# Optimization experiments

Measured on AMD Instinct MI355X. Metric: run time of the kernel, lower is better.

Reference implementation:

```python
import jax, jax.numpy as jnp
import numpy as np

K = 16          # num neighbor samples
SHARE = 8       # share_planes


def _conv1x1(x, w, b=None):
    # x: [B, Cin, N, K], w: [Cout, Cin]
    y = jnp.einsum('oc,bcnk->bonk', w, x)
    if b is not None:
        y = y + b[None, :, None, None]
    return y


def setup_inputs() -> dict:
    key = jax.random.key(0)
    ks = jax.random.split(key, 18)
    B, CIN, N = 4, 64, 16384
    MID, OUT, PT = 64, 128, 8
    s = 0.05  # weight scale

    def w(k, shape):
        return jax.random.normal(k, shape, jnp.float32) * s

    return {
        'sm_feats': jax.random.normal(ks[0], (B, CIN, N, K), jnp.float32),
        'sm_ppfs': jax.random.normal(ks[1], (B, PT, N, K), jnp.float32),
        'w0': w(ks[2], (OUT, CIN)),   'b0': w(ks[3], (OUT,)),
        'w1': w(ks[4], (MID, OUT)),   'b1': w(ks[5], (MID,)),
        'w2': w(ks[6], (MID, OUT)),   'b2': w(ks[7], (MID,)),
        'w3': w(ks[8], (MID, OUT)),   'b3': w(ks[9], (MID,)),
        'pw1': w(ks[10], (MID, PT)),
        'pw2': w(ks[11], (MID, MID)),
        'cw1': w(ks[12], (MID // SHARE, MID * K)),
        'cw2': w(ks[13], (K * MID // SHARE, MID // SHARE)), 'cb2': w(ks[14], (K * MID // SHARE,)),
        'wout': w(ks[15], (OUT, MID)), 'bout': w(ks[16], (OUT,)),
    }


def reference(sm_feats, sm_ppfs, w0, b0, w1, b1, w2, b2, w3, b3,
              pw1, pw2, cw1, cw2, cb2, wout, bout):
    B, _, N, k = sm_feats.shape
    xn = jax.nn.relu(_conv1x1(sm_feats, w0, b0))          # [B, OUT, N, K]
    x = xn[:, :, :, 0:1]                                   # [B, OUT, N, 1]
    identity = x
    x1 = _conv1x1(x, w1, b1)                               # [B, MID, N, 1]
    x2 = _conv1x1(xn, w2, b2)                              # [B, MID, N, K]
    x3 = _conv1x1(xn, w3, b3)                              # [B, MID, N, K]
    ptf = _conv1x1(jax.nn.relu(_conv1x1(sm_ppfs, pw1)), pw2)  # [B, MID, N, K]
    x3 = x3 + ptf
    xfs = x1 - x2 + ptf                                    # [B, MID, N, K]
    mid = xfs.shape[1]
    # transpose(2,3).view(B, MID*K, 1, N)
    xfs = jnp.transpose(xfs, (0, 1, 3, 2)).reshape(B, mid * k, 1, N)
    h = jax.nn.relu(_conv1x1(xfs, cw1))                    # [B, MID//S, 1, N]
    wl = _conv1x1(h, cw2, cb2)                             # [B, K*MID//S, 1, N]
    wl = wl.reshape(B, mid // SHARE, k, N)
    w = jax.nn.softmax(wl, axis=2)                         # softmax over K samples
    w = jnp.transpose(w, (0, 1, 3, 2))                     # [B, MID//S, N, K]
    w = jnp.tile(w, (1, SHARE, 1, 1))                      # [B, MID, N, K]
    out = jax.nn.relu(jnp.sum(w * x3, axis=3, keepdims=True))  # [B, MID, N, 1]
    out = _conv1x1(out, wout, bout) + identity             # [B, OUT, N, 1]
    return out[:, :, :, 0]                                 # [B, OUT, N]
```

## Files before the change

kernel.cpp:

```cpp
#include <hip/hip_runtime.h>
#include <stdint.h>

typedef unsigned int uint32;
typedef __attribute__((ext_vector_type(4))) float f32x4;
typedef __attribute__((ext_vector_type(4))) uint32 u32x4;
typedef __attribute__((ext_vector_type(8))) short bf16x8;

#define NPOS_TOTAL 65536
#define WPB 4
#define POS_PER_WAVE 32
#define NBLOCKS 512
#define CSTRIDE 262144

#define OFF_AW0 0
#define OFF_W2N 4096
#define OFF_W3 8192
#define OFF_PW1 12288
#define OFF_PW2 13312
#define N_LDS_TAB 15360
#define OFF_CW1 15360
#define OFF_W1 19456
#define OFF_CW2 23552
#define OFF_WOUT 24064

__device__ __forceinline__ uint32 pack_bf16(float lo, float hi) {
  uint32 a = __builtin_bit_cast(uint32, lo);
  uint32 b = __builtin_bit_cast(uint32, hi);
  return ((b + 0x8000u) & 0xffff0000u) | ((a + 0x8000u) >> 16);
}
__device__ __forceinline__ float bf_lo(uint32 u) { return __builtin_bit_cast(float, u << 16); }
__device__ __forceinline__ float bf_hi(uint32 u) { return __builtin_bit_cast(float, u & 0xffff0000u); }
__device__ __forceinline__ float bcast(float v, int l) {
  return __builtin_bit_cast(float, __builtin_amdgcn_readlane(__builtin_bit_cast(int, v), l));
}
__device__ __forceinline__ uint32 cvt_pk(float lo, float hi) {
  uint32 r;
  asm("v_cvt_pk_bf16_f32 %0, %1, %2" : "=v"(r) : "v"(lo), "v"(hi));
  return r;
}
__device__ __forceinline__ uint32 bperm(int addr, uint32 src) {
  return (uint32)__builtin_amdgcn_ds_bpermute(addr, (int)src);
}
__device__ __forceinline__ float bpermf(int addr, float src) {
  return __builtin_bit_cast(float,
      __builtin_amdgcn_ds_bpermute(addr, __builtin_bit_cast(int, src)));
}
__device__ __forceinline__ f32x4 mfma16(u32x4 a, u32x4 b, f32x4 c) {
  return __builtin_amdgcn_mfma_f32_16x16x32_bf16(
      __builtin_bit_cast(bf16x8, a), __builtin_bit_cast(bf16x8, b), c, 0, 0, 0);
}
__device__ __forceinline__ f32x4 relu4(f32x4 v) {
  f32x4 r;
  r[0] = fmaxf(v[0], 0.f);
  r[1] = fmaxf(v[1], 0.f);
  r[2] = fmaxf(v[2], 0.f);
  r[3] = fmaxf(v[3], 0.f);
  return r;
}

__global__ void pack_weights_kernel(const float* __restrict__ w0, const float* __restrict__ w1,
                                    const float* __restrict__ w2, const float* __restrict__ w3,
                                    const float* __restrict__ pw1, const float* __restrict__ pw2,
                                    const float* __restrict__ cw1, const float* __restrict__ cw2,
                                    const float* __restrict__ wout, uint32* __restrict__ ws) {
  int t = threadIdx.x + blockIdx.x * blockDim.x;
  int stride = blockDim.x * gridDim.x;

  for (int i = t; i < 4096; i += stride) {
    int r = i & 3, l = (i >> 2) & 63, ts = i >> 8;
    int mt = ts >> 1, s = ts & 1;
    int o = mt * 16 + (l & 15);
    int c = s * 32 + ((l >> 4) << 3) + 2 * r;
    ws[OFF_AW0 + i] = pack_bf16(w0[o * 64 + c], w0[o * 64 + c + 1]);
  }
  for (int i = t; i < 4096; i += stride) {
    int r = i & 3, l = (i >> 2) & 63, ts = i >> 8;
    int nt = ts >> 2, s = ts & 3;
    int c = nt * 16 + (l & 15);
    int o = s * 32 + ((l >> 4) << 3) + 2 * r;
    ws[OFF_W2N + i] = pack_bf16(-w2[c * 128 + o], -w2[c * 128 + o + 1]);
    ws[OFF_W3 + i] = pack_bf16(w3[c * 128 + o], w3[c * 128 + o + 1]);
    ws[OFF_W1 + i] = pack_bf16(w1[c * 128 + o], w1[c * 128 + o + 1]);
  }
  for (int i = t; i < 1024; i += stride) {
    int r = i & 3, l = (i >> 2) & 63, nt = i >> 8;
    int m = nt * 16 + (l & 15);
    int qq = ((l >> 4) << 3) + 2 * r;
    float lo = (qq < 8) ? pw1[m * 8 + qq] : 0.f;
    float hi = (qq < 8) ? pw1[m * 8 + qq + 1] : 0.f;
    ws[OFF_PW1 + i] = pack_bf16(lo, hi);
  }
  for (int i = t; i < 2048; i += stride) {
    int r = i & 3, l = (i >> 2) & 63, ts = i >> 8;
    int nt = ts >> 1, s = ts & 1;
    int m2 = nt * 16 + (l & 15);
    int m = s * 32 + ((l >> 4) << 3) + 2 * r;
    ws[OFF_PW2 + i] = pack_bf16(pw2[m2 * 64 + m], pw2[m2 * 64 + m + 1]);
  }
  for (int i = t; i < 4096; i += stride) {
    int rr = i & 3, l = (i >> 2) & 63, th = i >> 8;
    int j = th >> 1, h = th & 1;
    int d = h * 4 + rr;
    int qq = l & 15, gg = l >> 4;
    int e0 = 2 * d, e1 = 2 * d + 1;
    int c0 = (e0 >> 2) * 16 + qq, k0 = gg * 4 + (e0 & 3);
    int c1 = (e1 >> 2) * 16 + qq, k1 = gg * 4 + (e1 & 3);
    ws[OFF_CW1 + i] = pack_bf16(cw1[j * 1024 + c0 * 16 + k0], cw1[j * 1024 + c1 * 16 + k1]);
  }
  for (int i = t; i < 512; i += stride) {
    int j = i >> 6, l2 = i & 63;
    ws[OFF_CW2 + i] = pack_bf16(cw2[l2 * 8 + j], cw2[(l2 + 64) * 8 + j]);
  }
  for (int i = t; i < 4096; i += stride) {
    int c = i >> 6, o2 = i & 63;
    ws[OFF_WOUT + i] = pack_bf16(wout[o2 * 64 + c], wout[(o2 + 64) * 64 + c]);
  }
}

__launch_bounds__(256, 2)
__global__ void pt_mfma(const float* __restrict__ feats, const float* __restrict__ ppfs,
                        const float* __restrict__ b0, const float* __restrict__ b1,
                        const float* __restrict__ b2, const float* __restrict__ b3,
                        const float* __restrict__ cb2, const float* __restrict__ bout,
                        const uint32* __restrict__ ws, float* __restrict__ out) {
  __shared__ uint32 sT[N_LDS_TAB];
  __shared__ float sId[WPB][128];

  const int tid = threadIdx.x;
  {
    u32x4* dst = (u32x4*)sT;
    const u32x4* src = (const u32x4*)ws;
#pragma unroll 1
    for (int i = tid; i < N_LDS_TAB / 4; i += 256) dst[i] = src[i];
  }
  __syncthreads();

  const int lane = tid & 63;
  const int wv = tid >> 6;
  const int q = lane & 15;
  const int g = lane >> 4;
  const bool isLo = (lane < 32);
  const bool qlo = ((q & 4) == 0);

  const int addrLo = 4 * (q + 16 * ((2 * g) & 3));
  const int addrHi = 4 * (q + 16 * ((2 * g + 1) & 3));
  const int addrC0 = 4 * (16 * g);
  const int addrI0 = 4 * ((q & 3) * 16 + 4 * g);

  f32x4 b0f[8];
#pragma unroll
  for (int mt = 0; mt < 8; mt++) b0f[mt] = *(const f32x4*)(b0 + mt * 16 + 4 * g);
  float bfsF[4], b3F[4];
#pragma unroll
  for (int nt = 0; nt < 4; nt++) {
    bfsF[nt] = b1[nt * 16 + q] - b2[nt * 16 + q];
    b3F[nt] = b3[nt * 16 + q];
  }
  const float cb2A = cb2[lane], cb2B = cb2[lane + 64];
  const float boutA = bout[lane], boutB = bout[lane + 64];

  float* idp = &sId[wv][0];

  const int wgid = blockIdx.x * WPB + wv;
  const int p0 = wgid * POS_PER_WAVE;

  int zoff = 0;

#pragma unroll 1
  for (int pi = 0; pi < POS_PER_WAVE; ++pi) {
    asm volatile("" : "+v"(zoff));
    const int p = p0 + pi;
    const int b = p >> 14, npos = p & 16383;

    const u32x4* gcw1_4 = (const u32x4*)(ws + OFF_CW1) + zoff;
    const u32x4* gw1_4 = (const u32x4*)(ws + OFF_W1) + zoff;
    const uint32* gcw2p = ws + OFF_CW2 + zoff;
    const uint32* gwoutp = ws + OFF_WOUT + zoff;

    u32x4 fB[2];
    {
      const float* fbase = feats + (size_t)(b * 64) * CSTRIDE + npos * 16 + q;
#pragma unroll
      for (int s = 0; s < 2; s++) {
#pragma unroll
        for (int t2 = 0; t2 < 4; t2++) {
          int c0 = s * 32 + 8 * g + 2 * t2;
          float v0 = fbase[c0 * CSTRIDE];
          float v1 = fbase[c0 * CSTRIDE + CSTRIDE];
          fB[s][t2] = cvt_pk(v0, v1);
        }
      }
    }

    u32x4 ppA = {0u, 0u, 0u, 0u};
    if (g == 0) {
      const float* pbase = ppfs + (size_t)(b * 8) * CSTRIDE + npos * 16 + q;
      float pv[8];
#pragma unroll
      for (int j = 0; j < 8; j++) pv[j] = pbase[j * CSTRIDE];
#pragma unroll
      for (int t2 = 0; t2 < 4; t2++) ppA[t2] = cvt_pk(pv[2 * t2], pv[2 * t2 + 1]);
    }

    f32x4 xnD[8];
#pragma unroll
    for (int mt = 0; mt < 8; mt++) {
      f32x4 acc = b0f[mt];
#pragma unroll
      for (int s = 0; s < 2; s++) {
        u32x4 aw = *(const u32x4*)&sT[OFF_AW0 + ((mt * 2 + s) * 64 + lane) * 4 + zoff];
        acc = mfma16(aw, fB[s], acc);
      }
      xnD[mt] = relu4(acc);
    }

    if (q == 0) {
#pragma unroll
      for (int mt = 0; mt < 8; mt++) *(f32x4*)(idp + mt * 16 + 4 * g) = xnD[mt];
    }

    u32x4 XNB[4];
#pragma unroll
    for (int s = 0; s < 4; s++) {
      uint32 dA0 = cvt_pk(xnD[2 * s][0], xnD[2 * s][1]);
      uint32 dA1 = cvt_pk(xnD[2 * s][2], xnD[2 * s][3]);
      uint32 dB0 = cvt_pk(xnD[2 * s + 1][0], xnD[2 * s + 1][1]);
      uint32 dB1 = cvt_pk(xnD[2 * s + 1][2], xnD[2 * s + 1][3]);
      uint32 pa, pb;
      pa = bperm(addrLo, dA0); pb = bperm(addrLo, dB0); XNB[s][0] = isLo ? pa : pb;
      pa = bperm(addrLo, dA1); pb = bperm(addrLo, dB1); XNB[s][1] = isLo ? pa : pb;
      pa = bperm(addrHi, dA0); pb = bperm(addrHi, dB0); XNB[s][2] = isLo ? pa : pb;
      pa = bperm(addrHi, dA1); pb = bperm(addrHi, dB1); XNB[s][3] = isLo ? pa : pb;
    }

    u32x4 xc0[4];
#pragma unroll
    for (int s = 0; s < 4; s++) {
#pragma unroll
      for (int r = 0; r < 4; r++) xc0[s][r] = bperm(addrC0, XNB[s][r]);
    }

    f32x4 tD[4];
#pragma unroll
    for (int nt = 0; nt < 4; nt++) {
      f32x4 z = {0.f, 0.f, 0.f, 0.f};
      u32x4 bw = *(const u32x4*)&sT[OFF_PW1 + (nt * 64 + lane) * 4 + zoff];
      tD[nt] = relu4(mfma16(ppA, bw, z));
    }
    u32x4 tA[2];
#pragma unroll
    for (int s = 0; s < 2; s++) {
      uint32 dA0 = cvt_pk(tD[2 * s][0], tD[2 * s][1]);
      uint32 dA1 = cvt_pk(tD[2 * s][2], tD[2 * s][3]);
      uint32 dB0 = cvt_pk(tD[2 * s + 1][0], tD[2 * s + 1][1]);
      uint32 dB1 = cvt_pk(tD[2 * s + 1][2], tD[2 * s + 1][3]);
      uint32 pa, pb;
      pa = bperm(addrLo, dA0); pb = bperm(addrLo, dB0); tA[s][0] = isLo ? pa : pb;
      pa = bperm(addrLo, dA1); pb = bperm(addrLo, dB1); tA[s][1] = isLo ? pa : pb;
      pa = bperm(addrHi, dA0); pb = bperm(addrHi, dB0); tA[s][2] = isLo ? pa : pb;
      pa = bperm(addrHi, dA1); pb = bperm(addrHi, dB1); tA[s][3] = isLo ? pa : pb;
    }
    f32x4 ptfD[4];
#pragma unroll
    for (int nt = 0; nt < 4; nt++) {
      f32x4 acc = {0.f, 0.f, 0.f, 0.f};
#pragma unroll
      for (int s = 0; s < 2; s++) {
        u32x4 bw = *(const u32x4*)&sT[OFF_PW2 + ((nt * 2 + s) * 64 + lane) * 4 + zoff];
        acc = mfma16(tA[s], bw, acc);
      }
      ptfD[nt] = acc;
    }

    f32x4 xfs[4], x3v[4];
#pragma unroll
    for (int nt = 0; nt < 4; nt++) {
      f32x4 acc = {bfsF[nt], bfsF[nt], bfsF[nt], bfsF[nt]};
#pragma unroll
      for (int s = 0; s < 4; s++) {
        u32x4 bw = *(const u32x4*)&sT[OFF_W2N + ((nt * 4 + s) * 64 + lane) * 4 + zoff];
        acc = mfma16(XNB[s], bw, acc);
      }
#pragma unroll
      for (int s = 0; s < 4; s++) {
        u32x4 bw = gw1_4[(nt * 4 + s) * 64 + lane];
        acc = mfma16(xc0[s], bw, acc);
      }
      xfs[nt] = acc + ptfD[nt];

      f32x4 acc3 = {b3F[nt], b3F[nt], b3F[nt], b3F[nt]};
#pragma unroll
      for (int s = 0; s < 4; s++) {
        u32x4 bw = *(const u32x4*)&sT[OFF_W3 + ((nt * 4 + s) * 64 + lane) * 4 + zoff];
        acc3 = mfma16(XNB[s], bw, acc3);
      }
      x3v[nt] = acc3 + ptfD[nt];
    }

    float hp[8];
#pragma unroll
    for (int j = 0; j < 8; j++) {
      float acc = 0.f;
#pragma unroll
      for (int h = 0; h < 2; h++) {
        u32x4 cwv = gcw1_4[(j * 2 + h) * 64 + lane];
#pragma unroll
        for (int rr = 0; rr < 4; rr++) {
          const int d = h * 4 + rr;
          const int nt = d >> 1;
          const int rb = (2 * d) & 3;
          acc = fmaf(bf_lo(cwv[rr]), xfs[nt][rb], acc);
          acc = fmaf(bf_hi(cwv[rr]), xfs[nt][rb + 1], acc);
        }
      }
      hp[j] = acc;
    }
#pragma unroll
    for (int j = 0; j < 8; j++) {
      float v = hp[j];
#pragma unroll
      for (int s = 1; s < 64; s <<= 1) v += __shfl_xor(v, s, 64);
      hp[j] = fmaxf(v, 0.f);
    }

    float wlA = cb2A, wlB = cb2B;
#pragma unroll
    for (int j = 0; j < 8; j++) {
      uint32 wp = gcw2p[j * 64 + lane];
      wlA = fmaf(bf_lo(wp), hp[j], wlA);
      wlB = fmaf(bf_hi(wp), hp[j], wlB);
    }

    float mA = wlA, mB = wlB;
#pragma unroll
    for (int s = 1; s < 16; s <<= 1) {
      mA = fmaxf(mA, __shfl_xor(mA, s, 64));
      mB = fmaxf(mB, __shfl_xor(mB, s, 64));
    }
    float eA = __expf(wlA - mA), eB = __expf(wlB - mB);
    float sA = eA, sB = eB;
#pragma unroll
    for (int s = 1; s < 16; s <<= 1) {
      sA += __shfl_xor(sA, s, 64);
      sB += __shfl_xor(sB, s, 64);
    }
    float smA = eA / sA, smB = eB / sB;

    float wI[4];
#pragma unroll
    for (int r = 0; r < 4; r++) {
      float wa = bpermf(addrI0 + 4 * r, smA);
      float wb = bpermf(addrI0 + 4 * r, smB);
      wI[r] = qlo ? wa : wb;
    }
    float om[4];
#pragma unroll
    for (int nt = 0; nt < 4; nt++) {
      float acc_o = 0.f;
#pragma unroll
      for (int r = 0; r < 4; r++) acc_o = fmaf(wI[r], x3v[nt][r], acc_o);
      acc_o += __shfl_xor(acc_o, 16, 64);
      acc_o += __shfl_xor(acc_o, 32, 64);
      om[nt] = fmaxf(acc_o, 0.f);
    }

    float outA = boutA + idp[lane];
    float outB = boutB + idp[lane + 64];
#pragma unroll
    for (int c = 0; c < 64; c++) {
      uint32 wp = gwoutp[c * 64 + lane];
      float sv = bcast(om[c >> 4], c & 15);
      outA = fmaf(bf_lo(wp), sv, outA);
      outB = fmaf(bf_hi(wp), sv, outB);
    }
    out[(size_t)(b * 128 + lane) * 16384 + npos] = outA;
    out[(size_t)(b * 128 + lane + 64) * 16384 + npos] = outB;
  }
}

extern "C" void kernel_launch(void* const* d_in, const int* in_sizes, int n_in,
                              void* d_out, int out_size, void* d_ws, size_t ws_size,
                              hipStream_t stream) {
  const float* feats = (const float*)d_in[0];
  const float* ppfs = (const float*)d_in[1];
  const float* w0 = (const float*)d_in[2];
  const float* b0 = (const float*)d_in[3];
  const float* w1 = (const float*)d_in[4];
  const float* b1 = (const float*)d_in[5];
  const float* w2 = (const float*)d_in[6];
  const float* b2 = (const float*)d_in[7];
  const float* w3 = (const float*)d_in[8];
  const float* b3 = (const float*)d_in[9];
  const float* pw1 = (const float*)d_in[10];
  const float* pw2 = (const float*)d_in[11];
  const float* cw1 = (const float*)d_in[12];
  const float* cw2 = (const float*)d_in[13];
  const float* cb2 = (const float*)d_in[14];
  const float* wout = (const float*)d_in[15];
  const float* bout = (const float*)d_in[16];
  (void)in_sizes; (void)n_in; (void)out_size; (void)ws_size;

  uint32* ws = (uint32*)d_ws;

  hipLaunchKernelGGL(pack_weights_kernel, dim3(8), dim3(256), 0, stream,
                     w0, w1, w2, w3, pw1, pw2, cw1, cw2, wout, ws);
  hipLaunchKernelGGL(pt_mfma, dim3(NBLOCKS), dim3(256), 0, stream,
                     feats, ppfs, b0, b1, b2, b3, cb2, bout, ws, (float*)d_out);
}
```

Before: 810.7 us.

## Prefetch next position's inputs, move W3 to global, vectorize output stores

```diff
diff --git a/kernel.cpp b/kernel.cpp
--- a/kernel.cpp
+++ b/kernel.cpp
@@ -8,16 +8,16 @@
 
 #define NPOS_TOTAL 65536
 #define WPB 4
-#define POS_PER_WAVE 32
-#define NBLOCKS 512
+#define POS_PER_WAVE 16
+#define NBLOCKS 1024
 #define CSTRIDE 262144
 
 #define OFF_AW0 0
 #define OFF_W2N 4096
-#define OFF_W3 8192
-#define OFF_PW1 12288
-#define OFF_PW2 13312
-#define N_LDS_TAB 15360
+#define OFF_PW1 8192
+#define OFF_PW2 9216
+#define N_LDS_TAB 11264
+#define OFF_W3G 11264
 #define OFF_CW1 15360
 #define OFF_W1 19456
 #define OFF_CW2 23552
@@ -79,7 +79,7 @@
     int c = nt * 16 + (l & 15);
     int o = s * 32 + ((l >> 4) << 3) + 2 * r;
     ws[OFF_W2N + i] = pack_bf16(-w2[c * 128 + o], -w2[c * 128 + o + 1]);
-    ws[OFF_W3 + i] = pack_bf16(w3[c * 128 + o], w3[c * 128 + o + 1]);
+    ws[OFF_W3G + i] = pack_bf16(w3[c * 128 + o], w3[c * 128 + o + 1]);
     ws[OFF_W1 + i] = pack_bf16(w1[c * 128 + o], w1[c * 128 + o + 1]);
   }
   for (int i = t; i < 1024; i += stride) {
@@ -112,12 +112,13 @@
     ws[OFF_CW2 + i] = pack_bf16(cw2[l2 * 8 + j], cw2[(l2 + 64) * 8 + j]);
   }
   for (int i = t; i < 4096; i += stride) {
-    int c = i >> 6, o2 = i & 63;
-    ws[OFF_WOUT + i] = pack_bf16(wout[o2 * 64 + c], wout[(o2 + 64) * 64 + c]);
-  }
-}
-
-__launch_bounds__(256, 2)
+    int r = i & 3, l = (i >> 2) & 63, c4 = i >> 8;
+    int c = 4 * c4 + r;
+    ws[OFF_WOUT + i] = pack_bf16(wout[l * 64 + c], wout[(l + 64) * 64 + c]);
+  }
+}
+
+__launch_bounds__(256, 3)
 __global__ void pt_mfma(const float* __restrict__ feats, const float* __restrict__ ppfs,
                         const float* __restrict__ b0, const float* __restrict__ b1,
                         const float* __restrict__ b2, const float* __restrict__ b3,
@@ -147,9 +148,6 @@
   const int addrC0 = 4 * (16 * g);
   const int addrI0 = 4 * ((q & 3) * 16 + 4 * g);
 
-  f32x4 b0f[8];
-#pragma unroll
-  for (int mt = 0; mt < 8; mt++) b0f[mt] = *(const f32x4*)(b0 + mt * 16 + 4 * g);
   float bfsF[4], b3F[4];
 #pragma unroll
   for (int nt = 0; nt < 4; nt++) {
@@ -157,7 +155,7 @@
     b3F[nt] = b3[nt * 16 + q];
   }
   const float cb2A = cb2[lane], cb2B = cb2[lane + 64];
-  const float boutA = bout[lane], boutB = bout[lane + 64];
+  const float boutA0 = bout[lane], boutB0 = bout[lane + 64];
 
   float* idp = &sId[wv][0];
 
@@ -165,6 +163,24 @@
   const int p0 = wgid * POS_PER_WAVE;
 
   int zoff = 0;
+
+  float fvA[16], pvA[8], fvB[16], pvB[8];
+  {
+    const int b = p0 >> 14, npos = p0 & 16383;
+    const float* fb = feats + (size_t)(b * 64) * CSTRIDE + npos * 16 + q;
+#pragma unroll
+    for (int s = 0; s < 2; s++)
+#pragma unroll
+      for (int u = 0; u < 8; u++)
+        fvA[s * 8 + u] = fb[(size_t)(s * 32 + 8 * g + u) * CSTRIDE];
+    if (g == 0) {
+      const float* pb = ppfs + (size_t)(b * 8) * CSTRIDE + npos * 16 + q;
+#pragma unroll
+      for (int j = 0; j < 8; j++) pvA[j] = pb[(size_t)j * CSTRIDE];
+    }
+  }
+
+  float oA0 = 0.f, oA1 = 0.f, oA2 = 0.f, oB0 = 0.f, oB1 = 0.f, oB2 = 0.f;
 
 #pragma unroll 1
   for (int pi = 0; pi < POS_PER_WAVE; ++pi) {
@@ -172,40 +188,46 @@
     const int p = p0 + pi;
     const int b = p >> 14, npos = p & 16383;
 
+    const bool havenext = (pi + 1 < POS_PER_WAVE);
+    if (havenext) {
+      const int pn = p + 1;
+      const int bn = pn >> 14, nn = pn & 16383;
+      const float* fb = feats + (size_t)(bn * 64) * CSTRIDE + nn * 16 + q;
+#pragma unroll
+      for (int s = 0; s < 2; s++)
+#pragma unroll
+        for (int u = 0; u < 8; u++)
+          fvB[s * 8 + u] = fb[(size_t)(s * 32 + 8 * g + u) * CSTRIDE];
+      if (g == 0) {
+        const float* pb = ppfs + (size_t)(bn * 8) * CSTRIDE + nn * 16 + q;
+#pragma unroll
+        for (int j = 0; j < 8; j++) pvB[j] = pb[(size_t)j * CSTRIDE];
+      }
+    }
+
     const u32x4* gcw1_4 = (const u32x4*)(ws + OFF_CW1) + zoff;
     const u32x4* gw1_4 = (const u32x4*)(ws + OFF_W1) + zoff;
+    const u32x4* gw3_4 = (const u32x4*)(ws + OFF_W3G) + zoff;
+    const u32x4* gwout4 = (const u32x4*)(ws + OFF_WOUT) + zoff;
     const uint32* gcw2p = ws + OFF_CW2 + zoff;
-    const uint32* gwoutp = ws + OFF_WOUT + zoff;
 
     u32x4 fB[2];
-    {
-      const float* fbase = feats + (size_t)(b * 64) * CSTRIDE + npos * 16 + q;
-#pragma unroll
-      for (int s = 0; s < 2; s++) {
-#pragma unroll
-        for (int t2 = 0; t2 < 4; t2++) {
-          int c0 = s * 32 + 8 * g + 2 * t2;
-          float v0 = fbase[c0 * CSTRIDE];
-          float v1 = fbase[c0 * CSTRIDE + CSTRIDE];
-          fB[s][t2] = cvt_pk(v0, v1);
-        }
-      }
-    }
+#pragma unroll
+    for (int s = 0; s < 2; s++)
+#pragma unroll
+      for (int t2 = 0; t2 < 4; t2++)
+        fB[s][t2] = cvt_pk(fvA[s * 8 + 2 * t2], fvA[s * 8 + 2 * t2 + 1]);
 
     u32x4 ppA = {0u, 0u, 0u, 0u};
     if (g == 0) {
-      const float* pbase = ppfs + (size_t)(b * 8) * CSTRIDE + npos * 16 + q;
-      float pv[8];
-#pragma unroll
-      for (int j = 0; j < 8; j++) pv[j] = pbase[j * CSTRIDE];
-#pragma unroll
-      for (int t2 = 0; t2 < 4; t2++) ppA[t2] = cvt_pk(pv[2 * t2], pv[2 * t2 + 1]);
+#pragma unroll
+      for (int t2 = 0; t2 < 4; t2++) ppA[t2] = cvt_pk(pvA[2 * t2], pvA[2 * t2 + 1]);
     }
 
     f32x4 xnD[8];
 #pragma unroll
     for (int mt = 0; mt < 8; mt++) {
-      f32x4 acc = b0f[mt];
+      f32x4 acc = *(const f32x4*)(b0 + mt * 16 + 4 * g);
 #pragma unroll
       for (int s = 0; s < 2; s++) {
         u32x4 aw = *(const u32x4*)&sT[OFF_AW0 + ((mt * 2 + s) * 64 + lane) * 4 + zoff];
@@ -291,7 +313,7 @@
       f32x4 acc3 = {b3F[nt], b3F[nt], b3F[nt], b3F[nt]};
 #pragma unroll
       for (int s = 0; s < 4; s++) {
-        u32x4 bw = *(const u32x4*)&sT[OFF_W3 + ((nt * 4 + s) * 64 + lane) * 4 + zoff];
+        u32x4 bw = gw3_4[(nt * 4 + s) * 64 + lane];
         acc3 = mfma16(XNB[s], bw, acc3);
       }
       x3v[nt] = acc3 + ptfD[nt];
@@ -364,17 +386,39 @@
       om[nt] = fmaxf(acc_o, 0.f);
     }
 
-    float outA = boutA + idp[lane];
-    float outB = boutB + idp[lane + 64];
-#pragma unroll
-    for (int c = 0; c < 64; c++) {
-      uint32 wp = gwoutp[c * 64 + lane];
-      float sv = bcast(om[c >> 4], c & 15);
-      outA = fmaf(bf_lo(wp), sv, outA);
-      outB = fmaf(bf_hi(wp), sv, outB);
-    }
-    out[(size_t)(b * 128 + lane) * 16384 + npos] = outA;
-    out[(size_t)(b * 128 + lane + 64) * 16384 + npos] = outB;
+    float outA = boutA0 + idp[lane];
+    float outB = boutB0 + idp[lane + 64];
+#pragma unroll
+    for (int c4 = 0; c4 < 16; c4++) {
+      u32x4 wp4 = gwout4[c4 * 64 + lane];
+#pragma unroll
+      for (int r = 0; r < 4; r++) {
+        float sv = bcast(om[c4 >> 2], (4 * c4 + r) & 15);
+        outA = fmaf(bf_lo(wp4[r]), sv, outA);
+        outB = fmaf(bf_hi(wp4[r]), sv, outB);
+      }
+    }
+
+    const int ph = pi & 3;
+    if (ph == 0) { oA0 = outA; oB0 = outB; }
+    else if (ph == 1) { oA1 = outA; oB1 = outB; }
+    else if (ph == 2) { oA2 = outA; oB2 = outB; }
+    else {
+      f32x4 vA, vB;
+      vA[0] = oA0; vA[1] = oA1; vA[2] = oA2; vA[3] = outA;
+      vB[0] = oB0; vB[1] = oB1; vB[2] = oB2; vB[3] = outB;
+      *(f32x4*)(out + (size_t)(b * 128 + lane) * 16384 + (npos - 3)) = vA;
+      *(f32x4*)(out + (size_t)(b * 128 + lane + 64) * 16384 + (npos - 3)) = vB;
+    }
+
+    if (havenext) {
+#pragma unroll
+      for (int i = 0; i < 16; i++) fvA[i] = fvB[i];
+      if (g == 0) {
+#pragma unroll
+        for (int j = 0; j < 8; j++) pvA[j] = pvB[j];
+      }
+    }
   }
 }
 
```

Result: slower. 1.396 ms (+72.2%).
